# Kernel optimization log

Hardware: AMD Instinct MI355X
Metric: run time of the kernel (lower is better)

Reference implementation:

```python
import jax, jax.numpy as jnp
import numpy as np

_EPS = 1e-06


def setup_inputs() -> dict:
    key = jax.random.key(0)
    k1, k2, k3, k4, k5 = jax.random.split(key, 5)
    B, N = 2, 8192
    return {
        "kp_before": jax.random.normal(k1, (B, N, 3), dtype=jnp.float32),
        "kp_warped_pred": jax.random.normal(k2, (B, N, 3), dtype=jnp.float32),
        "pose_gt": jax.random.normal(k3, (B, 3, 4), dtype=jnp.float32),
        "overlap_weights": jax.random.uniform(k4, (B, N), dtype=jnp.float32),
        "inlier_logits": jax.random.normal(k5, (B, N), dtype=jnp.float32),
    }


def _bce_with_logits(x, z):
    # elementwise BCEWithLogits: z*softplus(-x) + (1-z)*softplus(x)
    return z * jax.nn.softplus(-x) + (1.0 - z) * jax.nn.softplus(x)


def _balanced_loss(logits, label):
    # BalancedLoss: mean BCE within each of the 2 label groups, averaged over groups
    bce = _bce_with_logits(logits, label)
    loss = jnp.float32(0.0)
    for i in range(2):
        mask = (label == i).astype(jnp.float32)
        cnt = jnp.sum(mask)
        group = jnp.where(cnt > 0, jnp.sum(bce * mask) / jnp.maximum(cnt, 1.0), 0.0)
        loss = loss + group / 2.0
    return loss


def reference(kp_before, kp_warped_pred, pose_gt, overlap_weights, inlier_logits):
    B, N, _ = kp_before.shape
    M = B * N
    # se3_transform_list: warped_gt[b] = kp_before[b] @ R[b]^T + t[b]
    R = pose_gt[:, :, :3]            # [B,3,3]
    t = pose_gt[:, :, 3]             # [B,3]
    kp_warped_gt = jnp.einsum('bij,bnj->bni', R, kp_before) + t[:, None, :]
    # torch.cat(list, dim=0) over equal-sized chunks == reshape
    pred = kp_warped_pred.reshape(M, 3)
    gt = kp_warped_gt.reshape(M, 3)
    corr_err = pred - gt               # [M,3]
    # pairwise L2 distance matrix [M,M] (O(N^2) traffic) + 1-NN argmin
    sq = (jnp.sum(pred * pred, axis=1)[:, None]
          + jnp.sum(gt * gt, axis=1)[None, :]
          - 2.0 * (pred @ gt.T))
    dist_map = jnp.sqrt(jnp.maximum(sq, 0.0))
    knn_ind = jnp.argmin(dist_map, axis=1)
    binary_mask = (knn_ind == jnp.arange(M)).astype(jnp.float32)
    inlier_err = _balanced_loss(inlier_logits.reshape(M), binary_mask)
    # metric == 'mae'
    err = jnp.sum(jnp.abs(corr_err), axis=-1)  # [M]
    w = overlap_weights.reshape(M)
    mean_err = jnp.sum(w * err) / jnp.maximum(jnp.sum(w), _EPS)
    return mean_err + inlier_err
```

## Files before the change

kernel.cpp:

```cpp
#include <hip/hip_runtime.h>
#include <cstdint>

#define TPB 256
#define IT 8
#define JCHUNK 64

__global__ void prep_kernel(const float* __restrict__ kp_before,
                            const float* __restrict__ pred,
                            const float* __restrict__ pose,
                            float4* __restrict__ gt4,
                            float* __restrict__ thr,
                            unsigned int* __restrict__ good,
                            float* __restrict__ accum,
                            int M, int N) {
    int tid = blockIdx.x * blockDim.x + threadIdx.x;
    if (tid < 8) accum[tid] = 0.0f;
    int stride = gridDim.x * blockDim.x;
    for (int i = tid; i < M; i += stride) {
        good[i] = 0u;
        int b = i / N;
        const float* P = pose + b * 12;
        float k0 = kp_before[3*i+0];
        float k1 = kp_before[3*i+1];
        float k2 = kp_before[3*i+2];
        float g0 = fmaf(P[2],  k2, fmaf(P[1], k1, P[0]*k0)) + P[3];
        float g1 = fmaf(P[6],  k2, fmaf(P[5], k1, P[4]*k0)) + P[7];
        float g2 = fmaf(P[10], k2, fmaf(P[9], k1, P[8]*k0)) + P[11];
        float sg;
        {
            #pragma clang fp contract(off)
            sg = (g0*g0 + g1*g1) + g2*g2;
        }
        gt4[i] = make_float4(g0, g1, g2, sg);

        float p0 = pred[3*i+0], p1 = pred[3*i+1], p2 = pred[3*i+2];
        float sp;
        {
            #pragma clang fp contract(off)
            sp = (p0*p0 + p1*p1) + p2*p2;
        }
        float t0 = 2.0f*p0, t1 = 2.0f*p1, t2 = 2.0f*p2;
        float dot2 = fmaf(t2, g2, fmaf(t1, g1, t0*g0));
        float v = (sp + sg) - dot2;
        thr[i] = fmaxf(v, 0.0f);
    }
}

__global__ void __launch_bounds__(TPB, 8) flags_kernel(
        const float* __restrict__ pred,
        const float4* __restrict__ gt4,
        const float* __restrict__ thr,
        unsigned int* __restrict__ good,
        int M, int numI) {
    __shared__ float4 sh[JCHUNK];
    int ic = blockIdx.x % numI;
    int jc = blockIdx.x / numI;
    int j0 = jc * JCHUNK;
    int jmax = M - j0; if (jmax > JCHUNK) jmax = JCHUNK;

    for (int k = threadIdx.x; k < jmax; k += TPB) {
        sh[k] = gt4[j0 + k];
    }
    __syncthreads();

    float tp0[IT], tp1[IT], tp2[IT], sp[IT], m[IT];
    int ibase = ic * (TPB * IT) + threadIdx.x;
    #pragma unroll
    for (int k = 0; k < IT; k++) {
        int i = ibase + k * TPB;
        if (i >= M) i = M - 1;
        float p0 = pred[3*i+0], p1 = pred[3*i+1], p2 = pred[3*i+2];
        {
            #pragma clang fp contract(off)
            sp[k] = (p0*p0 + p1*p1) + p2*p2;
        }
        tp0[k] = 2.0f * p0;
        tp1[k] = 2.0f * p1;
        tp2[k] = 2.0f * p2;
        m[k] = __uint_as_float(0x7f7fffffu);
    }

    int j = 0;
    for (; j + 1 < jmax; j += 2) {
        float4 ga = sh[j];
        float4 gb = sh[j + 1];
        #pragma unroll
        for (int k = 0; k < IT; k++) {
            float va = (sp[k] + ga.w) -
                       fmaf(tp2[k], ga.z, fmaf(tp1[k], ga.y, tp0[k] * ga.x));
            float vb = (sp[k] + gb.w) -
                       fmaf(tp2[k], gb.z, fmaf(tp1[k], gb.y, tp0[k] * gb.x));
            m[k] = fminf(fminf(va, vb), m[k]);
        }
    }
    if (j < jmax) {
        float4 ga = sh[j];
        #pragma unroll
        for (int k = 0; k < IT; k++) {
            float va = (sp[k] + ga.w) -
                       fmaf(tp2[k], ga.z, fmaf(tp1[k], ga.y, tp0[k] * ga.x));
            m[k] = fminf(va, m[k]);
        }
    }

    int j1 = j0 + jmax;
    #pragma unroll
    for (int k = 0; k < IT; k++) {
        int i = ibase + k * TPB;
        if (i >= M) continue;
        float dii = thr[i];
        float vminc = fmaxf(m[k], 0.0f);
        bool bad;
        if (i >= j1) {
            bad = (vminc <= dii);
        } else {
            bad = (vminc < dii);
            if (!bad && i > j0) {
                int je = i < j1 ? (i - j0) : jmax;
                for (int jj = 0; jj < je; jj++) {
                    float4 g = sh[jj];
                    float v = (sp[k] + g.w) -
                              fmaf(tp2[k], g.z, fmaf(tp1[k], g.y, tp0[k] * g.x));
                    if (fmaxf(v, 0.0f) <= dii) { bad = true; break; }
                }
            }
        }
        if (!bad) atomicAdd(&good[i], 1u);
    }
}

__device__ inline float wave_red(float v) {
    #pragma unroll
    for (int off = 32; off > 0; off >>= 1) v += __shfl_down(v, off, 64);
    return v;
}

__global__ void finalize_kernel(const float* __restrict__ pred,
                                const float4* __restrict__ gt4,
                                const float* __restrict__ ow,
                                const float* __restrict__ logits,
                                const unsigned int* __restrict__ good,
                                float* __restrict__ accum, int M, int numJ) {
    float werr = 0.f, wsum = 0.f, b1 = 0.f, c1 = 0.f, b0 = 0.f, c0 = 0.f;
    int stride = gridDim.x * blockDim.x;
    for (int i = blockIdx.x * blockDim.x + threadIdx.x; i < M; i += stride) {
        float x = logits[i];
        float l1p = log1pf(expf(-fabsf(x)));
        if (good[i] == (unsigned int)numJ) {
            b1 += fmaxf(-x, 0.f) + l1p; c1 += 1.f;
        } else {
            b0 += fmaxf(x, 0.f) + l1p;  c0 += 1.f;
        }
        float4 g = gt4[i];
        float p0 = pred[3*i+0], p1 = pred[3*i+1], p2 = pred[3*i+2];
        float e = (fabsf(p0 - g.x) + fabsf(p1 - g.y)) + fabsf(p2 - g.z);
        float wi = ow[i];
        werr += wi * e;
        wsum += wi;
    }
    werr = wave_red(werr); wsum = wave_red(wsum);
    b1 = wave_red(b1); c1 = wave_red(c1);
    b0 = wave_red(b0); c0 = wave_red(c0);
    if ((threadIdx.x & 63) == 0) {
        atomicAdd(&accum[0], werr);
        atomicAdd(&accum[1], wsum);
        atomicAdd(&accum[2], b1);
        atomicAdd(&accum[3], c1);
        atomicAdd(&accum[4], b0);
        atomicAdd(&accum[5], c0);
    }
}

__global__ void scalar_kernel(const float* __restrict__ accum,
                              float* __restrict__ out) {
    float mean_err = accum[0] / fmaxf(accum[1], 1e-6f);
    float g1 = (accum[3] > 0.f) ? (accum[2] / fmaxf(accum[3], 1.f)) : 0.f;
    float g0 = (accum[5] > 0.f) ? (accum[4] / fmaxf(accum[5], 1.f)) : 0.f;
    out[0] = mean_err + (g0 * 0.5f + g1 * 0.5f);
}

extern "C" void kernel_launch(void* const* d_in, const int* in_sizes, int n_in,
                              void* d_out, int out_size, void* d_ws, size_t ws_size,
                              hipStream_t stream) {
    const float* kp_before = (const float*)d_in[0];
    const float* pred      = (const float*)d_in[1];
    const float* pose      = (const float*)d_in[2];
    const float* ow        = (const float*)d_in[3];
    const float* logits    = (const float*)d_in[4];
    float* out = (float*)d_out;

    int M = in_sizes[3];
    int B = in_sizes[2] / 12;
    int N = M / B;

    char* ws = (char*)d_ws;
    float4* gt4 = (float4*)ws;
    float* thr = (float*)(ws + (size_t)M * 16);
    unsigned int* good = (unsigned int*)(ws + (size_t)M * 20);
    float* accum = (float*)(ws + (size_t)M * 24);

    int prep_blocks = (M + TPB - 1) / TPB;
    hipLaunchKernelGGL(prep_kernel, dim3(prep_blocks), dim3(TPB), 0, stream,
                       kp_before, pred, pose, gt4, thr, good, accum, M, N);

    int numI = (M + TPB * IT - 1) / (TPB * IT);
    int numJ = (M + JCHUNK - 1) / JCHUNK;
    hipLaunchKernelGGL(flags_kernel, dim3(numI * numJ), dim3(TPB), 0, stream,
                       pred, gt4, thr, good, M, numI);

    hipLaunchKernelGGL(finalize_kernel, dim3(64), dim3(TPB), 0, stream,
                       pred, gt4, ow, logits, good, accum, M, numJ);

    hipLaunchKernelGGL(scalar_kernel, dim3(1), dim3(1), 0, stream,
                       accum, out);
}
```

Before: 122.6 us.

## Fuse prep, flags and finalize into one kernel with last-block reduction

```diff
diff --git a/kernel.cpp b/kernel.cpp
--- a/kernel.cpp
+++ b/kernel.cpp
@@ -3,67 +3,54 @@
 
 #define TPB 256
 #define IT 8
-#define JCHUNK 64
+#define JCHUNK 128
 
-__global__ void prep_kernel(const float* __restrict__ kp_before,
-                            const float* __restrict__ pred,
-                            const float* __restrict__ pose,
-                            float4* __restrict__ gt4,
-                            float* __restrict__ thr,
-                            unsigned int* __restrict__ good,
-                            float* __restrict__ accum,
-                            int M, int N) {
-    int tid = blockIdx.x * blockDim.x + threadIdx.x;
-    if (tid < 8) accum[tid] = 0.0f;
-    int stride = gridDim.x * blockDim.x;
-    for (int i = tid; i < M; i += stride) {
-        good[i] = 0u;
-        int b = i / N;
-        const float* P = pose + b * 12;
-        float k0 = kp_before[3*i+0];
-        float k1 = kp_before[3*i+1];
-        float k2 = kp_before[3*i+2];
-        float g0 = fmaf(P[2],  k2, fmaf(P[1], k1, P[0]*k0)) + P[3];
-        float g1 = fmaf(P[6],  k2, fmaf(P[5], k1, P[4]*k0)) + P[7];
-        float g2 = fmaf(P[10], k2, fmaf(P[9], k1, P[8]*k0)) + P[11];
-        float sg;
-        {
-            #pragma clang fp contract(off)
-            sg = (g0*g0 + g1*g1) + g2*g2;
-        }
-        gt4[i] = make_float4(g0, g1, g2, sg);
-
-        float p0 = pred[3*i+0], p1 = pred[3*i+1], p2 = pred[3*i+2];
-        float sp;
-        {
-            #pragma clang fp contract(off)
-            sp = (p0*p0 + p1*p1) + p2*p2;
-        }
-        float t0 = 2.0f*p0, t1 = 2.0f*p1, t2 = 2.0f*p2;
-        float dot2 = fmaf(t2, g2, fmaf(t1, g1, t0*g0));
-        float v = (sp + sg) - dot2;
-        thr[i] = fmaxf(v, 0.0f);
+__device__ __forceinline__ float4 compute_gt(const float* __restrict__ kp,
+                                             const float* __restrict__ P) {
+    float k0 = kp[0], k1 = kp[1], k2 = kp[2];
+    float g0 = fmaf(P[2],  k2, fmaf(P[1], k1, P[0]*k0)) + P[3];
+    float g1 = fmaf(P[6],  k2, fmaf(P[5], k1, P[4]*k0)) + P[7];
+    float g2 = fmaf(P[10], k2, fmaf(P[9], k1, P[8]*k0)) + P[11];
+    float sg;
+    {
+        #pragma clang fp contract(off)
+        sg = (g0*g0 + g1*g1) + g2*g2;
     }
+    return make_float4(g0, g1, g2, sg);
 }
 
-__global__ void __launch_bounds__(TPB, 8) flags_kernel(
+__device__ __forceinline__ float wave_red(float v) {
+    #pragma unroll
+    for (int off = 32; off > 0; off >>= 1) v += __shfl_down(v, off, 64);
+    return v;
+}
+
+__global__ void __launch_bounds__(TPB, 4) fused_kernel(
+        const float* __restrict__ kp,
         const float* __restrict__ pred,
-        const float4* __restrict__ gt4,
-        const float* __restrict__ thr,
+        const float* __restrict__ pose,
+        const float* __restrict__ ow,
+        const float* __restrict__ logits,
         unsigned int* __restrict__ good,
-        int M, int numI) {
+        unsigned int* __restrict__ done,
+        float* __restrict__ out,
+        int M, int N, int numI, int numJ, int nblocks) {
     __shared__ float4 sh[JCHUNK];
+    __shared__ float red[4 * 6];
+    __shared__ unsigned int is_last;
+
     int ic = blockIdx.x % numI;
     int jc = blockIdx.x / numI;
     int j0 = jc * JCHUNK;
     int jmax = M - j0; if (jmax > JCHUNK) jmax = JCHUNK;
 
     for (int k = threadIdx.x; k < jmax; k += TPB) {
-        sh[k] = gt4[j0 + k];
+        int j = j0 + k;
+        sh[k] = compute_gt(kp + 3*j, pose + (j / N) * 12);
     }
     __syncthreads();
 
-    float tp0[IT], tp1[IT], tp2[IT], sp[IT], m[IT];
+    float tp0[IT], tp1[IT], tp2[IT], sp[IT], thr[IT], m[IT];
     int ibase = ic * (TPB * IT) + threadIdx.x;
     #pragma unroll
     for (int k = 0; k < IT; k++) {
@@ -77,6 +64,9 @@
         tp0[k] = 2.0f * p0;
         tp1[k] = 2.0f * p1;
         tp2[k] = 2.0f * p2;
+        float4 gi = compute_gt(kp + 3*i, pose + (i / N) * 12);
+        float dot2 = fmaf(tp2[k], gi.z, fmaf(tp1[k], gi.y, tp0[k] * gi.x));
+        thr[k] = fmaxf((sp[k] + gi.w) - dot2, 0.0f);
         m[k] = __uint_as_float(0x7f7fffffu);
     }
 
@@ -108,7 +98,7 @@
     for (int k = 0; k < IT; k++) {
         int i = ibase + k * TPB;
         if (i >= M) continue;
-        float dii = thr[i];
+        float dii = thr[k];
         float vminc = fmaxf(m[k], 0.0f);
         bool bad;
         if (i >= j1) {
@@ -116,7 +106,7 @@
         } else {
             bad = (vminc < dii);
             if (!bad && i > j0) {
-                int je = i < j1 ? (i - j0) : jmax;
+                int je = (i < j1 ? i : j1) - j0;
                 for (int jj = 0; jj < je; jj++) {
                     float4 g = sh[jj];
                     float v = (sp[k] + g.w) -
@@ -127,33 +117,31 @@
         }
         if (!bad) atomicAdd(&good[i], 1u);
     }
-}
 
-__device__ inline float wave_red(float v) {
-    #pragma unroll
-    for (int off = 32; off > 0; off >>= 1) v += __shfl_down(v, off, 64);
-    return v;
-}
+    __syncthreads();
+    if (threadIdx.x == 0) {
+        __threadfence();
+        unsigned int prev = atomicAdd(done, 1u);
+        is_last = (prev == (unsigned int)(nblocks - 1)) ? 1u : 0u;
+    }
+    __syncthreads();
+    if (!is_last) return;
+    __threadfence();
 
-__global__ void finalize_kernel(const float* __restrict__ pred,
-                                const float4* __restrict__ gt4,
-                                const float* __restrict__ ow,
-                                const float* __restrict__ logits,
-                                const unsigned int* __restrict__ good,
-                                float* __restrict__ accum, int M, int numJ) {
     float werr = 0.f, wsum = 0.f, b1 = 0.f, c1 = 0.f, b0 = 0.f, c0 = 0.f;
-    int stride = gridDim.x * blockDim.x;
-    for (int i = blockIdx.x * blockDim.x + threadIdx.x; i < M; i += stride) {
+    for (int i = threadIdx.x; i < M; i += TPB) {
+        unsigned int g = __hip_atomic_load(&good[i], __ATOMIC_RELAXED,
+                                           __HIP_MEMORY_SCOPE_AGENT);
         float x = logits[i];
         float l1p = log1pf(expf(-fabsf(x)));
-        if (good[i] == (unsigned int)numJ) {
+        if (g == (unsigned int)numJ) {
             b1 += fmaxf(-x, 0.f) + l1p; c1 += 1.f;
         } else {
             b0 += fmaxf(x, 0.f) + l1p;  c0 += 1.f;
         }
-        float4 g = gt4[i];
+        float4 gg = compute_gt(kp + 3*i, pose + (i / N) * 12);
         float p0 = pred[3*i+0], p1 = pred[3*i+1], p2 = pred[3*i+2];
-        float e = (fabsf(p0 - g.x) + fabsf(p1 - g.y)) + fabsf(p2 - g.z);
+        float e = (fabsf(p0 - gg.x) + fabsf(p1 - gg.y)) + fabsf(p2 - gg.z);
         float wi = ow[i];
         werr += wi * e;
         wsum += wi;
@@ -161,56 +149,48 @@
     werr = wave_red(werr); wsum = wave_red(wsum);
     b1 = wave_red(b1); c1 = wave_red(c1);
     b0 = wave_red(b0); c0 = wave_red(c0);
+    int wid = threadIdx.x >> 6;
     if ((threadIdx.x & 63) == 0) {
-        atomicAdd(&accum[0], werr);
-        atomicAdd(&accum[1], wsum);
-        atomicAdd(&accum[2], b1);
-        atomicAdd(&accum[3], c1);
-        atomicAdd(&accum[4], b0);
-        atomicAdd(&accum[5], c0);
+        red[wid*6+0] = werr; red[wid*6+1] = wsum;
+        red[wid*6+2] = b1;   red[wid*6+3] = c1;
+        red[wid*6+4] = b0;   red[wid*6+5] = c0;
     }
-}
-
-__global__ void scalar_kernel(const float* __restrict__ accum,
-                              float* __restrict__ out) {
-    float mean_err = accum[0] / fmaxf(accum[1], 1e-6f);
-    float g1 = (accum[3] > 0.f) ? (accum[2] / fmaxf(accum[3], 1.f)) : 0.f;
-    float g0 = (accum[5] > 0.f) ? (accum[4] / fmaxf(accum[5], 1.f)) : 0.f;
-    out[0] = mean_err + (g0 * 0.5f + g1 * 0.5f);
+    __syncthreads();
+    if (threadIdx.x == 0) {
+        float t[6];
+        #pragma unroll
+        for (int q = 0; q < 6; q++)
+            t[q] = red[q] + red[6+q] + red[12+q] + red[18+q];
+        float mean_err = t[0] / fmaxf(t[1], 1e-6f);
+        float g1v = (t[3] > 0.f) ? (t[2] / fmaxf(t[3], 1.f)) : 0.f;
+        float g0v = (t[5] > 0.f) ? (t[4] / fmaxf(t[5], 1.f)) : 0.f;
+        out[0] = mean_err + (g0v * 0.5f + g1v * 0.5f);
+    }
 }
 
 extern "C" void kernel_launch(void* const* d_in, const int* in_sizes, int n_in,
                               void* d_out, int out_size, void* d_ws, size_t ws_size,
                               hipStream_t stream) {
-    const float* kp_before = (const float*)d_in[0];
-    const float* pred      = (const float*)d_in[1];
-    const float* pose      = (const float*)d_in[2];
-    const float* ow        = (const float*)d_in[3];
-    const float* logits    = (const float*)d_in[4];
+    const float* kp     = (const float*)d_in[0];
+    const float* pred   = (const float*)d_in[1];
+    const float* pose   = (const float*)d_in[2];
+    const float* ow     = (const float*)d_in[3];
+    const float* logits = (const float*)d_in[4];
     float* out = (float*)d_out;
 
     int M = in_sizes[3];
     int B = in_sizes[2] / 12;
     int N = M / B;
 
-    char* ws = (char*)d_ws;
-    float4* gt4 = (float4*)ws;
-    float* thr = (float*)(ws + (size_t)M * 16);
-    unsigned int* good = (unsigned int*)(ws + (size_t)M * 20);
-    float* accum = (float*)(ws + (size_t)M * 24);
+    unsigned int* good = (unsigned int*)d_ws;
+    unsigned int* done = (unsigned int*)((char*)d_ws + (size_t)M * 4);
 
-    int prep_blocks = (M + TPB - 1) / TPB;
-    hipLaunchKernelGGL(prep_kernel, dim3(prep_blocks), dim3(TPB), 0, stream,
-                       kp_before, pred, pose, gt4, thr, good, accum, M, N);
+    hipMemsetAsync(d_ws, 0, (size_t)M * 4 + 16, stream);
 
     int numI = (M + TPB * IT - 1) / (TPB * IT);
     int numJ = (M + JCHUNK - 1) / JCHUNK;
-    hipLaunchKernelGGL(flags_kernel, dim3(numI * numJ), dim3(TPB), 0, stream,
-                       pred, gt4, thr, good, M, numI);
-
-    hipLaunchKernelGGL(finalize_kernel, dim3(64), dim3(TPB), 0, stream,
-                       pred, gt4, ow, logits, good, accum, M, numJ);
-
-    hipLaunchKernelGGL(scalar_kernel, dim3(1), dim3(1), 0, stream,
-                       accum, out);
+    int nblocks = numI * numJ;
+    hipLaunchKernelGGL(fused_kernel, dim3(nblocks), dim3(TPB), 0, stream,
+                       kp, pred, pose, ow, logits, good, done, out,
+                       M, N, numI, numJ, nblocks);
 }
```

Measured after the change: 191.0 us. 1.56x slower.
